# Optimization experiments

Measured on AMD Instinct MI355X. Metric: run time of the kernel, lower is better.

## Reference

```python
import jax, jax.numpy as jnp
import numpy as np

HIDDEN = 512
INPUT = 256
P_VALUE = 0.2
EPS = 0.001


def setup_inputs() -> dict:
    key = jax.random.key(0)
    k1, k2, k3, k4 = jax.random.split(key, 4)
    stdv = 1.0 / np.sqrt(HIDDEN)
    inputs = jax.random.normal(k1, (64, 1024, INPUT), dtype=jnp.float32)
    weight_ih = jax.random.uniform(k2, (3 * HIDDEN, INPUT), jnp.float32, -stdv, stdv)
    weight_hh = jax.random.uniform(k3, (3 * HIDDEN, HIDDEN), jnp.float32, -stdv, stdv)
    bias = jax.random.uniform(k4, (3 * HIDDEN,), jnp.float32, -stdv, stdv)
    return {"inputs": inputs, "weight_ih": weight_ih, "weight_hh": weight_hh, "bias": bias}


def reference(inputs, weight_ih, weight_hh, bias):
    # inputs: [B, T, I] (batch_first). hidden=None -> h=c=0, k=-1.
    B, T, _ = inputs.shape
    H = weight_hh.shape[1]
    h0 = jnp.zeros((B, H), inputs.dtype)
    c0 = jnp.zeros((B, H), inputs.dtype)
    k0 = -jnp.ones((B, H), inputs.dtype)
    p_t = jnp.asarray(P_VALUE, inputs.dtype)  # learn_p=False: constant p

    def step(state, xt):
        h, c, k = state
        x, t = xt  # x: [B, I], t: scalar timestep
        gates = x @ weight_ih.T + h @ weight_hh.T + bias  # [B, 3H]
        r, o, g = jnp.split(gates, 3, axis=1)
        r = jax.nn.sigmoid(r)
        o = jax.nn.sigmoid(o)
        g = jnp.tanh(g)
        k_new = r * (t - EPS) + (1.0 - r) * k
        f = jnp.power((t - k_new + EPS) / (t - k_new + 1.0), p_t)
        c_new = f * c + (1.0 - f) * g
        h_new = o * jnp.tanh(c_new)
        return (h_new, c_new, k_new), h_new

    ts = jnp.arange(T, dtype=inputs.dtype)
    xs = jnp.transpose(inputs, (1, 0, 2))  # [T, B, I]
    (h_f, c_f, k_f), hs = jax.lax.scan(step, (h0, c0, k0), (xs, ts))
    out = jnp.transpose(hs, (1, 0, 2))  # [B, T, H]
    return out, h_f, c_f, k_f
```

## Files before the change

### kernel.cpp

```cpp
#include <hip/hip_runtime.h>
#include <stdint.h>
#include <stddef.h>


#define Hh   512
#define Tt   1024
#define Bb   64
#define II   256
#define EPSc 0.001f
#define PV   0.2f

typedef unsigned long long u64;

__global__ __launch_bounds__(1024) void plr_init(u64* hbuf2) {
  int idx = blockIdx.x * blockDim.x + threadIdx.x;
  hbuf2[idx] = 0ull;
  hbuf2[idx + 32768] = 0ull;
}

__global__ __launch_bounds__(512, 2)
void plr_main(
    const float* __restrict__ x,
    const float* __restrict__ Wih,
    const float* __restrict__ Whh,
    const float* __restrict__ bias,
    float* __restrict__ out,
    u64* hbuf2)
{
  __shared__ float h_tile[8 * Hh];
  __shared__ float x_tile[2 * 8 * II];
  __shared__ float part[3264];

  const int tid = threadIdx.x;
  const int w   = tid >> 6;
  const int l   = tid & 63;
  const int jj  = l & 15;
  const int kc  = (w << 2) | ((l >> 4) & 3);
  const int bid = blockIdx.x;
  const int g   = bid & 7;
  const int s   = bid >> 3;
  const int j0  = s * 16;
  const int b0  = g * 8;

  float whh[3][16];
  float wih[3][8];
#pragma unroll
  for (int gi = 0; gi < 3; ++gi) {
    const int row = gi * Hh + j0 + jj;
    const float4* ph = (const float4*)(Whh + (size_t)row * Hh + kc * 16);
#pragma unroll
    for (int i = 0; i < 4; ++i) {
      float4 v = ph[i];
      whh[gi][4*i+0] = v.x; whh[gi][4*i+1] = v.y;
      whh[gi][4*i+2] = v.z; whh[gi][4*i+3] = v.w;
    }
    const float4* pi = (const float4*)(Wih + (size_t)row * II + kc * 8);
#pragma unroll
    for (int i = 0; i < 2; ++i) {
      float4 v = pi[i];
      wih[gi][4*i+0] = v.x; wih[gi][4*i+1] = v.y;
      wih[gi][4*i+2] = v.z; wih[gi][4*i+3] = v.w;
    }
  }

  float c_st = 0.0f, k_st = -1.0f;
  float bia0 = 0.f, bia1 = 0.f, bia2 = 0.f;
  if (tid < 128) {
    const int jr = tid & 15;
    bia0 = bias[0 * Hh + j0 + jr];
    bia1 = bias[1 * Hh + j0 + jr];
    bia2 = bias[2 * Hh + j0 + jr];
  }

  {
    const int bl = tid >> 6, k4 = (tid & 63) * 4;
    *(float4*)(x_tile + bl * II + k4) =
        *(const float4*)(x + ((size_t)(b0 + bl) * Tt + 0) * II + k4);
  }
  __syncthreads();

  bool broken = false;

  for (int t = 0; t < Tt; ++t) {
    const u64* hb = hbuf2 + (size_t)(t & 1) * Bb * Hh + (size_t)b0 * Hh;
    u64 got[8];
#pragma unroll
    for (int i = 0; i < 8; ++i)
      got[i] = __hip_atomic_load(hb + (size_t)i * Hh + tid, __ATOMIC_RELAXED,
                                 __HIP_MEMORY_SCOPE_AGENT);

    const float* xt = x_tile + (t & 1) * 8 * II;
    float xacc[3][8];
#pragma unroll
    for (int bl = 0; bl < 8; ++bl) {
      const float4* x4 = (const float4*)(xt + bl * II) + kc * 2;
      float a0 = 0.f, a1 = 0.f, a2 = 0.f;
#pragma unroll
      for (int i = 0; i < 2; ++i) {
        float4 xv = x4[i];
        a0 = fmaf(wih[0][4*i+0], xv.x, a0); a0 = fmaf(wih[0][4*i+1], xv.y, a0);
        a0 = fmaf(wih[0][4*i+2], xv.z, a0); a0 = fmaf(wih[0][4*i+3], xv.w, a0);
        a1 = fmaf(wih[1][4*i+0], xv.x, a1); a1 = fmaf(wih[1][4*i+1], xv.y, a1);
        a1 = fmaf(wih[1][4*i+2], xv.z, a1); a1 = fmaf(wih[1][4*i+3], xv.w, a1);
        a2 = fmaf(wih[2][4*i+0], xv.x, a2); a2 = fmaf(wih[2][4*i+1], xv.y, a2);
        a2 = fmaf(wih[2][4*i+2], xv.z, a2); a2 = fmaf(wih[2][4*i+3], xv.w, a2);
      }
      xacc[0][bl] = a0; xacc[1][bl] = a1; xacc[2][bl] = a2;
    }

    {
      const unsigned want = (unsigned)t;
      int it = 0;
      for (;;) {
        bool ok = true;
#pragma unroll
        for (int i = 0; i < 8; ++i) ok &= ((unsigned)(got[i] >> 32) == want);
        if (__all((int)ok)) break;
        if (++it > (1 << 20)) { broken = true; break; }
        __builtin_amdgcn_s_sleep(1);
#pragma unroll
        for (int i = 0; i < 8; ++i)
          if ((unsigned)(got[i] >> 32) != want)
            got[i] = __hip_atomic_load(hb + (size_t)i * Hh + tid,
                                       __ATOMIC_RELAXED,
                                       __HIP_MEMORY_SCOPE_AGENT);
      }
    }

#pragma unroll
    for (int i = 0; i < 8; ++i)
      h_tile[i * Hh + tid] = __uint_as_float((unsigned)got[i]);
    __syncthreads();

#pragma unroll
    for (int pass = 0; pass < 2; ++pass) {
      float acc[3][4];
#pragma unroll
      for (int b4 = 0; b4 < 4; ++b4) {
        const int bl = pass * 4 + b4;
        const float4* h4 = (const float4*)(h_tile + bl * Hh) + kc * 4;
        float a0 = xacc[0][bl], a1 = xacc[1][bl], a2 = xacc[2][bl];
#pragma unroll
        for (int i = 0; i < 4; ++i) {
          float4 hv = h4[i];
          a0 = fmaf(whh[0][4*i+0], hv.x, a0); a0 = fmaf(whh[0][4*i+1], hv.y, a0);
          a0 = fmaf(whh[0][4*i+2], hv.z, a0); a0 = fmaf(whh[0][4*i+3], hv.w, a0);
          a1 = fmaf(whh[1][4*i+0], hv.x, a1); a1 = fmaf(whh[1][4*i+1], hv.y, a1);
          a1 = fmaf(whh[1][4*i+2], hv.z, a1); a1 = fmaf(whh[1][4*i+3], hv.w, a1);
          a2 = fmaf(whh[2][4*i+0], hv.x, a2); a2 = fmaf(whh[2][4*i+1], hv.y, a2);
          a2 = fmaf(whh[2][4*i+2], hv.z, a2); a2 = fmaf(whh[2][4*i+3], hv.w, a2);
        }
        acc[0][b4] = a0; acc[1][b4] = a1; acc[2][b4] = a2;
      }
#pragma unroll
      for (int gi = 0; gi < 3; ++gi)
#pragma unroll
        for (int b4 = 0; b4 < 4; ++b4) {
          float v = acc[gi][b4];
          v += __shfl_xor(v, 16, 64);
          v += __shfl_xor(v, 32, 64);
          if (l < 16)
            part[((gi * 8 + pass * 4 + b4) * 8 + w) * 17 + jj] = v;
        }
    }

    if (t + 1 < Tt) {
      const int bl = tid >> 6, k4 = (tid & 63) * 4;
      *(float4*)(x_tile + ((t + 1) & 1) * 8 * II + bl * II + k4) =
          *(const float4*)(x + ((size_t)(b0 + bl) * Tt + (t + 1)) * II + k4);
    }
    __syncthreads();

    if (tid < 128) {
      const int jr = tid & 15, br = tid >> 4;
      float s0 = bia0, s1 = bia1, s2 = bia2;
#pragma unroll
      for (int ww = 0; ww < 8; ++ww) {
        s0 += part[((0 * 8 + br) * 8 + ww) * 17 + jr];
        s1 += part[((1 * 8 + br) * 8 + ww) * 17 + jr];
        s2 += part[((2 * 8 + br) * 8 + ww) * 17 + jr];
      }
      const float tf = (float)t;
      const float r  = 1.0f / (1.0f + __expf(-s0));
      const float o  = 1.0f / (1.0f + __expf(-s1));
      const float gg = 1.0f - 2.0f / (1.0f + __expf(2.0f * s2));
      const float kn = r * (tf - EPSc) + (1.0f - r) * k_st;
      const float d  = tf - kn;
      const float f  = __expf(PV * __logf((d + EPSc) / (d + 1.0f)));
      const float cn = f * c_st + (1.0f - f) * gg;
      const float hn = o * (1.0f - 2.0f / (1.0f + __expf(2.0f * cn)));
      c_st = cn; k_st = kn;

      if (t + 1 < Tt) {
        u64* hp = hbuf2 + (size_t)((t + 1) & 1) * Bb * Hh +
                  (size_t)(b0 + br) * Hh + j0 + jr;
        u64 atom = ((u64)(unsigned)(t + 1) << 32) |
                   (u64)__float_as_uint(hn);
        __hip_atomic_store(hp, atom, __ATOMIC_RELAXED,
                           __HIP_MEMORY_SCOPE_AGENT);
      }

      const int b = b0 + br, j = j0 + jr;
      out[((size_t)b * Tt + t) * Hh + j] = hn;
      if (t == Tt - 1) {
        const size_t base = (size_t)Bb * Tt * Hh;
        out[base + 0 * Bb * Hh + (size_t)b * Hh + j] = hn;
        out[base + 1 * Bb * Hh + (size_t)b * Hh + j] = cn;
        out[base + 2 * Bb * Hh + (size_t)b * Hh + j] = kn;
      }
    }
  }
  (void)broken;
}

extern "C" void kernel_launch(void* const* d_in, const int* in_sizes, int n_in,
                              void* d_out, int out_size, void* d_ws, size_t ws_size,
                              hipStream_t stream) {
  const float* x    = (const float*)d_in[0];
  const float* Wih  = (const float*)d_in[1];
  const float* Whh  = (const float*)d_in[2];
  const float* bias = (const float*)d_in[3];
  float* out = (float*)d_out;

  u64* hbuf2 = (u64*)d_ws;

  plr_init<<<32, 1024, 0, stream>>>(hbuf2);
  plr_main<<<256, 512, 0, stream>>>(x, Wih, Whh, bias, out, hbuf2);
}
```

Baseline: 5.781 ms.

## Remove per-step h-tile barrier by giving each wave its own h and x slices

The loads of h and x into shared memory are remapped so that each wave fetches exactly the slice of h_tile and x_tile that it later reads itself. That makes the __syncthreads after the h_tile fill, and the one after the initial x load, unnecessary. The partial-sum buffer is double-buffered by timestep so the one remaining barrier per step still prevents write-after-read hazards with the reducer waves. The intent is to shorten the latency-bound serial recurrence step, at the cost of twice the shared memory for partials and a correctness argument that relies on wave-private ownership.

```diff
diff --git a/kernel.cpp b/kernel.cpp
--- a/kernel.cpp
+++ b/kernel.cpp
@@ -29,7 +29,7 @@
 {
   __shared__ float h_tile[8 * Hh];
   __shared__ float x_tile[2 * 8 * II];
-  __shared__ float part[3264];
+  __shared__ float part[2 * 3264];
 
   const int tid = threadIdx.x;
   const int w   = tid >> 6;
@@ -41,6 +41,9 @@
   const int s   = bid >> 3;
   const int j0  = s * 16;
   const int b0  = g * 8;
+  const int jw  = w << 6;
+  const int bls = l >> 3;
+  const int xk  = (w << 5) + (l & 7) * 4;
 
   float whh[3][16];
   float wih[3][8];
@@ -72,12 +75,8 @@
     bia2 = bias[2 * Hh + j0 + jr];
   }
 
-  {
-    const int bl = tid >> 6, k4 = (tid & 63) * 4;
-    *(float4*)(x_tile + bl * II + k4) =
-        *(const float4*)(x + ((size_t)(b0 + bl) * Tt + 0) * II + k4);
-  }
-  __syncthreads();
+  *(float4*)(x_tile + bls * II + xk) =
+      *(const float4*)(x + ((size_t)(b0 + bls) * Tt + 0) * II + xk);
 
   bool broken = false;
 
@@ -86,8 +85,8 @@
     u64 got[8];
 #pragma unroll
     for (int i = 0; i < 8; ++i)
-      got[i] = __hip_atomic_load(hb + (size_t)i * Hh + tid, __ATOMIC_RELAXED,
-                                 __HIP_MEMORY_SCOPE_AGENT);
+      got[i] = __hip_atomic_load(hb + (size_t)i * Hh + jw + l,
+                                 __ATOMIC_RELAXED, __HIP_MEMORY_SCOPE_AGENT);
 
     const float* xt = x_tile + (t & 1) * 8 * II;
     float xacc[3][8];
@@ -121,7 +120,7 @@
 #pragma unroll
         for (int i = 0; i < 8; ++i)
           if ((unsigned)(got[i] >> 32) != want)
-            got[i] = __hip_atomic_load(hb + (size_t)i * Hh + tid,
+            got[i] = __hip_atomic_load(hb + (size_t)i * Hh + jw + l,
                                        __ATOMIC_RELAXED,
                                        __HIP_MEMORY_SCOPE_AGENT);
       }
@@ -129,9 +128,9 @@
 
 #pragma unroll
     for (int i = 0; i < 8; ++i)
-      h_tile[i * Hh + tid] = __uint_as_float((unsigned)got[i]);
-    __syncthreads();
-
+      h_tile[i * Hh + jw + l] = __uint_as_float((unsigned)got[i]);
+
+    float* pb = part + (t & 1) * 3264;
 #pragma unroll
     for (int pass = 0; pass < 2; ++pass) {
       float acc[3][4];
@@ -160,15 +159,14 @@
           v += __shfl_xor(v, 16, 64);
           v += __shfl_xor(v, 32, 64);
           if (l < 16)
-            part[((gi * 8 + pass * 4 + b4) * 8 + w) * 17 + jj] = v;
+            pb[((gi * 8 + pass * 4 + b4) * 8 + w) * 17 + jj] = v;
         }
     }
 
-    if (t + 1 < Tt) {
-      const int bl = tid >> 6, k4 = (tid & 63) * 4;
-      *(float4*)(x_tile + ((t + 1) & 1) * 8 * II + bl * II + k4) =
-          *(const float4*)(x + ((size_t)(b0 + bl) * Tt + (t + 1)) * II + k4);
-    }
+    if (t + 1 < Tt)
+      *(float4*)(x_tile + ((t + 1) & 1) * 8 * II + bls * II + xk) =
+          *(const float4*)(x + ((size_t)(b0 + bls) * Tt + (t + 1)) * II + xk);
+
     __syncthreads();
 
     if (tid < 128) {
@@ -176,9 +174,9 @@
       float s0 = bia0, s1 = bia1, s2 = bia2;
 #pragma unroll
       for (int ww = 0; ww < 8; ++ww) {
-        s0 += part[((0 * 8 + br) * 8 + ww) * 17 + jr];
-        s1 += part[((1 * 8 + br) * 8 + ww) * 17 + jr];
-        s2 += part[((2 * 8 + br) * 8 + ww) * 17 + jr];
+        s0 += pb[((0 * 8 + br) * 8 + ww) * 17 + jr];
+        s1 += pb[((1 * 8 + br) * 8 + ww) * 17 + jr];
+        s2 += pb[((2 * 8 + br) * 8 + ww) * 17 + jr];
       }
       const float tf = (float)t;
       const float r  = 1.0f / (1.0f + __expf(-s0));
```

Measured after the change: 5.620 ms. 2.8% less time.
